# Kernel optimization log

Hardware: AMD Instinct MI355X
Metric: run time of the kernel (lower is better)

## Reference

```python
import jax, jax.numpy as jnp
import numpy as np

VOCAB, EMB, HID = 32000, 512, 1024
L, N = 512, 64


def setup_inputs() -> dict:
    key = jax.random.key(0)
    ks = jax.random.split(key, 10)
    d_in = HID + EMB
    s = 1.0 / np.sqrt(d_in)
    def lin(k):
        kw, kb = jax.random.split(k)
        W = jax.random.uniform(kw, (d_in, HID), jnp.float32, -s, s)
        b = jax.random.uniform(kb, (HID,), jnp.float32, -s, s)
        return W, b
    Wi, bi = lin(ks[0])
    Wf, bf = lin(ks[1])
    Wc, bc = lin(ks[2])
    Wo, bo = lin(ks[3])
    emb = jax.random.normal(ks[4], (VOCAB, EMB), jnp.float32)
    x = jax.random.randint(ks[5], (L, N), 0, VOCAB)
    return {"x": x, "emb": emb, "Wi": Wi, "bi": bi, "Wf": Wf, "bf": bf,
            "Wc": Wc, "bc": bc, "Wo": Wo, "bo": bo}


def reference(x, emb, Wi, bi, Wf, bf, Wc, bc, Wo, bo):
    # x: (L, N) int indices. Embed all timesteps up front (gather), then scan.
    xe = emb[x]  # (L, N, EMB)
    n = x.shape[1]
    h0 = jnp.zeros((n, HID), jnp.float32)
    c0 = jnp.zeros((n, HID), jnp.float32)

    def step(carry, xt):
        h, c = carry
        hx = jnp.concatenate([h, xt], axis=1)  # (N, HID+EMB)
        f = jax.nn.sigmoid(hx @ Wf + bf)
        i = jax.nn.sigmoid(hx @ Wi + bi)
        c_new = f * c + i * jnp.tanh(hx @ Wc + bc)
        o = jax.nn.sigmoid(hx @ Wo + bo)
        h_new = o * jnp.tanh(c_new)
        return (h_new, c_new), h_new

    (_, _), hs = jax.lax.scan(step, (h0, c0), xe)
    return hs  # (L, N, HID)
```

## Files before the change

### kernel.cpp

```cpp
#include <hip/hip_runtime.h>
#include <hip/hip_bf16.h>
#include <cstdint>
#include <cstddef>

typedef unsigned short u16;
typedef __attribute__((ext_vector_type(8))) short short8;
typedef __attribute__((ext_vector_type(4))) float f32x4;

#define L_SEQ 512
#define NB    64
#define HID_  1024
#define EMB_  512
#define DIN   1536
#define NKS   48
#define NKS_H 32
#define ARS   1544
#define HSEQ  (NB * HID_)

__device__ __forceinline__ u16 f2b(float f) {
    uint32_t u = __float_as_uint(f);
    u = (u + 0x7FFFu + ((u >> 16) & 1u)) >> 16;
    return (u16)u;
}

__global__ void pack_w_k(const float* __restrict__ Wi, const float* __restrict__ Wf,
                         const float* __restrict__ Wc, const float* __restrict__ Wo,
                         u16* __restrict__ whxp) {
    int b  = blockIdx.x;
    int ks = b % NKS;
    int gw = (b / NKS) & 3;
    int ug = b / (NKS * 4);
    const float* W = (gw == 0) ? Wi : (gw == 1) ? Wf : (gw == 2) ? Wc : Wo;
    int t  = threadIdx.x;
    int l  = t & 63;
    int ep = t >> 6;
    int k   = ks * 32 + ((l >> 4) * 8) + ep * 2;
    int col = ug * 16 + (l & 15);
    float v0 = W[(size_t)k * HID_ + col];
    float v1 = W[(size_t)(k + 1) * HID_ + col];
    uint32_t pk = (uint32_t)f2b(v0) | ((uint32_t)f2b(v1) << 16);
    size_t dst = (((size_t)b) * 64 + l) * 8 + (size_t)ep * 2;
    *(uint32_t*)(whxp + dst) = pk;
}

__global__ void zero_flags_k(uint32_t* __restrict__ flags) {
    flags[threadIdx.x] = 0u;
}

__global__ __launch_bounds__(256, 1) void lstm_persist_k(
    const u16* __restrict__ whxp, const float* __restrict__ emb,
    const int* __restrict__ x,
    const float* __restrict__ bi, const float* __restrict__ bf_,
    const float* __restrict__ bc, const float* __restrict__ bo,
    u16* __restrict__ hseq, uint32_t* __restrict__ flags,
    float* __restrict__ out)
{
    __shared__ __align__(16) u16 Atile[16][ARS];
    __shared__ float gbuf[4][16][17];

    const int tid = threadIdx.x;
    const int w   = tid >> 6;
    const int l   = tid & 63;
    const int ug  = blockIdx.x & 63;
    const int bj  = blockIdx.x >> 6;
    const int brow0 = bj * 16;

    short8 bw[NKS];
    {
        const short8* bp = (const short8*)whxp + ((size_t)(ug * 4 + w) * NKS) * 64 + l;
        #pragma unroll
        for (int ks = 0; ks < NKS; ++ks) bw[ks] = bp[ks * 64];
    }
    const float* bptr = (w == 0) ? bi : (w == 1) ? bf_ : (w == 2) ? bc : bo;
    const float bias = bptr[ug * 16 + (l & 15)];

    const int erow = tid >> 4;
    const int eu   = tid & 15;
    const size_t cidx = (size_t)(brow0 + erow) * HID_ + (size_t)ug * 16 + eu;
    float creg = 0.f;

    const int grow = tid >> 4;
    const int gc0  = (tid & 15) * 32;

    {
        int token = x[brow0 + grow];
        const float* es = emb + (size_t)token * EMB_ + gc0;
        #pragma unroll
        for (int j = 0; j < 4; ++j) {
            float4 a = *(const float4*)(es + j * 8);
            float4 b = *(const float4*)(es + j * 8 + 4);
            short8 v;
            v[0] = (short)f2b(a.x); v[1] = (short)f2b(a.y);
            v[2] = (short)f2b(a.z); v[3] = (short)f2b(a.w);
            v[4] = (short)f2b(b.x); v[5] = (short)f2b(b.y);
            v[6] = (short)f2b(b.z); v[7] = (short)f2b(b.w);
            *(short8*)(&Atile[grow][1024 + gc0 + j * 8]) = v;
        }
    }
    __syncthreads();

    for (int t = 0; t < L_SEQ; ++t) {
        f32x4 acc0 = {bias, bias, bias, bias};
        f32x4 acc1 = {0.f, 0.f, 0.f, 0.f};
        f32x4 acc2 = {0.f, 0.f, 0.f, 0.f};
        f32x4 acc3 = {0.f, 0.f, 0.f, 0.f};
        const u16* arow = &Atile[l & 15][(l >> 4) * 8];

        #pragma unroll
        for (int ks = NKS_H; ks < NKS; ks += 4) {
            acc0 = __builtin_amdgcn_mfma_f32_16x16x32_bf16(*(const short8*)(arow + ks * 32),        bw[ks],     acc0, 0, 0, 0);
            acc1 = __builtin_amdgcn_mfma_f32_16x16x32_bf16(*(const short8*)(arow + (ks + 1) * 32),  bw[ks + 1], acc1, 0, 0, 0);
            acc2 = __builtin_amdgcn_mfma_f32_16x16x32_bf16(*(const short8*)(arow + (ks + 2) * 32),  bw[ks + 2], acc2, 0, 0, 0);
            acc3 = __builtin_amdgcn_mfma_f32_16x16x32_bf16(*(const short8*)(arow + (ks + 3) * 32),  bw[ks + 3], acc3, 0, 0, 0);
        }
        if (t > 0) {
            #pragma unroll
            for (int ks = 0; ks < NKS_H; ks += 4) {
                acc0 = __builtin_amdgcn_mfma_f32_16x16x32_bf16(*(const short8*)(arow + ks * 32),        bw[ks],     acc0, 0, 0, 0);
                acc1 = __builtin_amdgcn_mfma_f32_16x16x32_bf16(*(const short8*)(arow + (ks + 1) * 32),  bw[ks + 1], acc1, 0, 0, 0);
                acc2 = __builtin_amdgcn_mfma_f32_16x16x32_bf16(*(const short8*)(arow + (ks + 2) * 32),  bw[ks + 2], acc2, 0, 0, 0);
                acc3 = __builtin_amdgcn_mfma_f32_16x16x32_bf16(*(const short8*)(arow + (ks + 3) * 32),  bw[ks + 3], acc3, 0, 0, 0);
            }
        }
        {
            int col = l & 15, rg = l >> 4;
            #pragma unroll
            for (int r = 0; r < 4; ++r)
                gbuf[w][rg * 4 + r][col] = (acc0[r] + acc1[r]) + (acc2[r] + acc3[r]);
        }
        __syncthreads();

        {
            float gi = gbuf[0][erow][eu];
            float gf = gbuf[1][erow][eu];
            float gc = gbuf[2][erow][eu];
            float go = gbuf[3][erow][eu];
            float fi = 1.f / (1.f + __expf(-gi));
            float ff = 1.f / (1.f + __expf(-gf));
            float fo = 1.f / (1.f + __expf(-go));
            float tc = 1.f - 2.f / (__expf(2.f * gc) + 1.f);
            float cn = ff * creg + fi * tc;
            float th = 1.f - 2.f / (__expf(2.f * cn) + 1.f);
            float hn = fo * th;
            creg = cn;
            out[(size_t)t * (NB * HID_) + cidx] = hn;
            __hip_atomic_store(hseq + (size_t)t * HSEQ + cidx, f2b(hn),
                               __ATOMIC_RELAXED, __HIP_MEMORY_SCOPE_AGENT);
        }

        if (t + 1 < L_SEQ) {
            asm volatile("s_waitcnt vmcnt(0)" ::: "memory");
            __syncthreads();
            if (tid == 0)
                __hip_atomic_store(&flags[bj * 64 + ug], (uint32_t)(t + 1),
                                   __ATOMIC_RELAXED, __HIP_MEMORY_SCOPE_AGENT);

            short8 xv[4];
            {
                int token = x[(t + 1) * NB + brow0 + grow];
                const float* es = emb + (size_t)token * EMB_ + gc0;
                #pragma unroll
                for (int j = 0; j < 4; ++j) {
                    float4 a = *(const float4*)(es + j * 8);
                    float4 b = *(const float4*)(es + j * 8 + 4);
                    short8 v;
                    v[0] = (short)f2b(a.x); v[1] = (short)f2b(a.y);
                    v[2] = (short)f2b(a.z); v[3] = (short)f2b(a.w);
                    v[4] = (short)f2b(b.x); v[5] = (short)f2b(b.y);
                    v[6] = (short)f2b(b.z); v[7] = (short)f2b(b.w);
                    xv[j] = v;
                }
            }

            if (tid < 64) {
                for (;;) {
                    uint32_t f = __hip_atomic_load(&flags[bj * 64 + tid],
                                                   __ATOMIC_RELAXED, __HIP_MEMORY_SCOPE_AGENT);
                    if (__all(f > (uint32_t)t)) break;
                    __builtin_amdgcn_s_sleep(2);
                }
            }
            __syncthreads();

            uint4 hv[8];
            {
                const uint32_t* hsrc = (const uint32_t*)(hseq + (size_t)t * HSEQ);
                #pragma unroll
                for (int it = 0; it < 8; ++it) {
                    int i = tid * 4 + it * 1024;
                    hv[it] = *(const uint4*)(hsrc + (size_t)(brow0 + (i >> 9)) * 512 + (i & 511));
                }
            }
            #pragma unroll
            for (int j = 0; j < 4; ++j)
                *(short8*)(&Atile[grow][1024 + gc0 + j * 8]) = xv[j];
            #pragma unroll
            for (int it = 0; it < 8; ++it) {
                int i = tid * 4 + it * 1024;
                *(uint4*)(&Atile[i >> 9][(i & 511) * 2]) = hv[it];
            }
            __syncthreads();
        }
    }
}

extern "C" void kernel_launch(void* const* d_in, const int* in_sizes, int n_in,
                              void* d_out, int out_size, void* d_ws, size_t ws_size,
                              hipStream_t stream) {
    const int*   x   = (const int*)d_in[0];
    const float* emb = (const float*)d_in[1];
    const float* Wi  = (const float*)d_in[2];
    const float* bi  = (const float*)d_in[3];
    const float* Wf  = (const float*)d_in[4];
    const float* bf  = (const float*)d_in[5];
    const float* Wc  = (const float*)d_in[6];
    const float* bc  = (const float*)d_in[7];
    const float* Wo  = (const float*)d_in[8];
    const float* bo  = (const float*)d_in[9];
    float* out = (float*)d_out;

    char* ws = (char*)d_ws;
    u16*      whxp  = (u16*)ws;
    uint32_t* flags = (uint32_t*)(ws + 12582912);
    u16*      hseq  = (u16*)(ws + 12582912 + 4096);

    pack_w_k<<<64 * 4 * NKS, 256, 0, stream>>>(Wi, Wf, Wc, Wo, whxp);
    zero_flags_k<<<1, 256, 0, stream>>>(flags);

    lstm_persist_k<<<256, 256, 0, stream>>>(whxp, emb, x, bi, bf, bc, bo,
                                            hseq, flags, out);
}
```

Before: 2.854 ms.

## Split K across waves, share A fragment across four gates, swizzle LDS

Each wave now owns a quarter of the K dimension for all four gates instead of one gate over full K. Each A fragment load from LDS feeds four MFMAs, which cuts LDS read traffic by four. The four partial sums are reduced through an enlarged gbuf, with bias added in the elementwise stage. The A tile uses an XOR swizzle instead of padding to avoid bank conflicts. The h part is zero-initialized and the t>0 skip is dropped, so step 0 does the full K. The embedding write is moved before the spin-wait, and the sleep interval is shortened.

```diff
diff --git a/kernel.cpp b/kernel.cpp
--- a/kernel.cpp
+++ b/kernel.cpp
@@ -11,10 +11,8 @@
 #define NB    64
 #define HID_  1024
 #define EMB_  512
-#define DIN   1536
 #define NKS   48
-#define NKS_H 32
-#define ARS   1544
+#define KQ_N  12
 #define HSEQ  (NB * HID_)
 
 __device__ __forceinline__ u16 f2b(float f) {
@@ -47,7 +45,9 @@
     flags[threadIdx.x] = 0u;
 }
 
-__global__ __launch_bounds__(256, 1) void lstm_persist_k(
+__global__ __launch_bounds__(256)
+__attribute__((amdgpu_waves_per_eu(1, 1)))
+void lstm_persist_k(
     const u16* __restrict__ whxp, const float* __restrict__ emb,
     const int* __restrict__ x,
     const float* __restrict__ bi, const float* __restrict__ bf_,
@@ -55,86 +55,104 @@
     u16* __restrict__ hseq, uint32_t* __restrict__ flags,
     float* __restrict__ out)
 {
-    __shared__ __align__(16) u16 Atile[16][ARS];
-    __shared__ float gbuf[4][16][17];
+    __shared__ __align__(16) u16 As[16 * 1536];
+    __shared__ float gbuf[4][4][16][16];
 
     const int tid = threadIdx.x;
-    const int w   = tid >> 6;
+    const int kq  = tid >> 6;
     const int l   = tid & 63;
     const int ug  = blockIdx.x & 63;
     const int bj  = blockIdx.x >> 6;
     const int brow0 = bj * 16;
 
-    short8 bw[NKS];
+    short8 bw0[KQ_N], bw1[KQ_N], bw2[KQ_N], bw3[KQ_N];
     {
-        const short8* bp = (const short8*)whxp + ((size_t)(ug * 4 + w) * NKS) * 64 + l;
-        #pragma unroll
-        for (int ks = 0; ks < NKS; ++ks) bw[ks] = bp[ks * 64];
+        const short8* bp = (const short8*)whxp + ((size_t)(ug * 4) * NKS) * 64 + l;
+        #pragma unroll
+        for (int j = 0; j < KQ_N; ++j) {
+            bw0[j] = bp[(0 * NKS + kq * KQ_N + j) * 64];
+            bw1[j] = bp[(1 * NKS + kq * KQ_N + j) * 64];
+            bw2[j] = bp[(2 * NKS + kq * KQ_N + j) * 64];
+            bw3[j] = bp[(3 * NKS + kq * KQ_N + j) * 64];
+        }
     }
-    const float* bptr = (w == 0) ? bi : (w == 1) ? bf_ : (w == 2) ? bc : bo;
-    const float bias = bptr[ug * 16 + (l & 15)];
+
+    const int arow = l & 15;
+    const int aq   = l >> 4;
+    const int k7   = arow & 7;
 
     const int erow = tid >> 4;
     const int eu   = tid & 15;
     const size_t cidx = (size_t)(brow0 + erow) * HID_ + (size_t)ug * 16 + eu;
+    const float bias_i = bi[ug * 16 + eu];
+    const float bias_f = bf_[ug * 16 + eu];
+    const float bias_c = bc[ug * 16 + eu];
+    const float bias_o = bo[ug * 16 + eu];
     float creg = 0.f;
 
     const int grow = tid >> 4;
-    const int gc0  = (tid & 15) * 32;
+    const int gx   = tid & 15;
 
     {
+        uint4 z = make_uint4(0u, 0u, 0u, 0u);
+        #pragma unroll
+        for (int it = 0; it < 8; ++it) {
+            int gidx = tid + it * 256;
+            int r_ = gidx >> 7, gr = gidx & 127;
+            *(uint4*)(&As[r_ * 1536 + (((gr ^ (r_ & 7))) << 3)]) = z;
+        }
         int token = x[brow0 + grow];
-        const float* es = emb + (size_t)token * EMB_ + gc0;
-        #pragma unroll
-        for (int j = 0; j < 4; ++j) {
-            float4 a = *(const float4*)(es + j * 8);
-            float4 b = *(const float4*)(es + j * 8 + 4);
+        const float* es = emb + (size_t)token * EMB_ + gx * 32;
+        #pragma unroll
+        for (int jj = 0; jj < 4; ++jj) {
+            float4 a = *(const float4*)(es + jj * 8);
+            float4 b = *(const float4*)(es + jj * 8 + 4);
             short8 v;
             v[0] = (short)f2b(a.x); v[1] = (short)f2b(a.y);
             v[2] = (short)f2b(a.z); v[3] = (short)f2b(a.w);
             v[4] = (short)f2b(b.x); v[5] = (short)f2b(b.y);
             v[6] = (short)f2b(b.z); v[7] = (short)f2b(b.w);
-            *(short8*)(&Atile[grow][1024 + gc0 + j * 8]) = v;
+            int gr = 128 + gx * 4 + jj;
+            *(short8*)(&As[grow * 1536 + ((gr ^ (grow & 7)) << 3)]) = v;
         }
     }
     __syncthreads();
 
     for (int t = 0; t < L_SEQ; ++t) {
-        f32x4 acc0 = {bias, bias, bias, bias};
-        f32x4 acc1 = {0.f, 0.f, 0.f, 0.f};
-        f32x4 acc2 = {0.f, 0.f, 0.f, 0.f};
-        f32x4 acc3 = {0.f, 0.f, 0.f, 0.f};
-        const u16* arow = &Atile[l & 15][(l >> 4) * 8];
-
-        #pragma unroll
-        for (int ks = NKS_H; ks < NKS; ks += 4) {
-            acc0 = __builtin_amdgcn_mfma_f32_16x16x32_bf16(*(const short8*)(arow + ks * 32),        bw[ks],     acc0, 0, 0, 0);
-            acc1 = __builtin_amdgcn_mfma_f32_16x16x32_bf16(*(const short8*)(arow + (ks + 1) * 32),  bw[ks + 1], acc1, 0, 0, 0);
-            acc2 = __builtin_amdgcn_mfma_f32_16x16x32_bf16(*(const short8*)(arow + (ks + 2) * 32),  bw[ks + 2], acc2, 0, 0, 0);
-            acc3 = __builtin_amdgcn_mfma_f32_16x16x32_bf16(*(const short8*)(arow + (ks + 3) * 32),  bw[ks + 3], acc3, 0, 0, 0);
-        }
-        if (t > 0) {
-            #pragma unroll
-            for (int ks = 0; ks < NKS_H; ks += 4) {
-                acc0 = __builtin_amdgcn_mfma_f32_16x16x32_bf16(*(const short8*)(arow + ks * 32),        bw[ks],     acc0, 0, 0, 0);
-                acc1 = __builtin_amdgcn_mfma_f32_16x16x32_bf16(*(const short8*)(arow + (ks + 1) * 32),  bw[ks + 1], acc1, 0, 0, 0);
-                acc2 = __builtin_amdgcn_mfma_f32_16x16x32_bf16(*(const short8*)(arow + (ks + 2) * 32),  bw[ks + 2], acc2, 0, 0, 0);
-                acc3 = __builtin_amdgcn_mfma_f32_16x16x32_bf16(*(const short8*)(arow + (ks + 3) * 32),  bw[ks + 3], acc3, 0, 0, 0);
-            }
+        f32x4 p0 = {0.f, 0.f, 0.f, 0.f};
+        f32x4 p1 = {0.f, 0.f, 0.f, 0.f};
+        f32x4 p2 = {0.f, 0.f, 0.f, 0.f};
+        f32x4 p3 = {0.f, 0.f, 0.f, 0.f};
+        #pragma unroll
+        for (int j = 0; j < KQ_N; ++j) {
+            int gr = (kq * KQ_N + j) * 4 + aq;
+            short8 av = *(const short8*)(&As[arow * 1536 + ((gr ^ k7) << 3)]);
+            p0 = __builtin_amdgcn_mfma_f32_16x16x32_bf16(av, bw0[j], p0, 0, 0, 0);
+            p1 = __builtin_amdgcn_mfma_f32_16x16x32_bf16(av, bw1[j], p1, 0, 0, 0);
+            p2 = __builtin_amdgcn_mfma_f32_16x16x32_bf16(av, bw2[j], p2, 0, 0, 0);
+            p3 = __builtin_amdgcn_mfma_f32_16x16x32_bf16(av, bw3[j], p3, 0, 0, 0);
         }
         {
             int col = l & 15, rg = l >> 4;
             #pragma unroll
-            for (int r = 0; r < 4; ++r)
-                gbuf[w][rg * 4 + r][col] = (acc0[r] + acc1[r]) + (acc2[r] + acc3[r]);
+            for (int r = 0; r < 4; ++r) {
+                gbuf[kq][0][rg * 4 + r][col] = p0[r];
+                gbuf[kq][1][rg * 4 + r][col] = p1[r];
+                gbuf[kq][2][rg * 4 + r][col] = p2[r];
+                gbuf[kq][3][rg * 4 + r][col] = p3[r];
+            }
         }
         __syncthreads();
 
         {
-            float gi = gbuf[0][erow][eu];
-            float gf = gbuf[1][erow][eu];
-            float gc = gbuf[2][erow][eu];
-            float go = gbuf[3][erow][eu];
+            float gi = ((gbuf[0][0][erow][eu] + gbuf[1][0][erow][eu]) +
+                        (gbuf[2][0][erow][eu] + gbuf[3][0][erow][eu])) + bias_i;
+            float gf = ((gbuf[0][1][erow][eu] + gbuf[1][1][erow][eu]) +
+                        (gbuf[2][1][erow][eu] + gbuf[3][1][erow][eu])) + bias_f;
+            float gc = ((gbuf[0][2][erow][eu] + gbuf[1][2][erow][eu]) +
+                        (gbuf[2][2][erow][eu] + gbuf[3][2][erow][eu])) + bias_c;
+            float go = ((gbuf[0][3][erow][eu] + gbuf[1][3][erow][eu]) +
+                        (gbuf[2][3][erow][eu] + gbuf[3][3][erow][eu])) + bias_o;
             float fi = 1.f / (1.f + __expf(-gi));
             float ff = 1.f / (1.f + __expf(-gf));
             float fo = 1.f / (1.f + __expf(-go));
@@ -155,49 +173,48 @@
                 __hip_atomic_store(&flags[bj * 64 + ug], (uint32_t)(t + 1),
                                    __ATOMIC_RELAXED, __HIP_MEMORY_SCOPE_AGENT);
 
-            short8 xv[4];
             {
                 int token = x[(t + 1) * NB + brow0 + grow];
-                const float* es = emb + (size_t)token * EMB_ + gc0;
-                #pragma unroll
-                for (int j = 0; j < 4; ++j) {
-                    float4 a = *(const float4*)(es + j * 8);
-                    float4 b = *(const float4*)(es + j * 8 + 4);
+                const float* es = emb + (size_t)token * EMB_ + gx * 32;
+                float4 ea[8];
+                #pragma unroll
+                for (int jj = 0; jj < 8; ++jj) ea[jj] = *(const float4*)(es + jj * 4);
+                #pragma unroll
+                for (int jj = 0; jj < 4; ++jj) {
+                    float4 a = ea[jj * 2], b = ea[jj * 2 + 1];
                     short8 v;
                     v[0] = (short)f2b(a.x); v[1] = (short)f2b(a.y);
                     v[2] = (short)f2b(a.z); v[3] = (short)f2b(a.w);
                     v[4] = (short)f2b(b.x); v[5] = (short)f2b(b.y);
                     v[6] = (short)f2b(b.z); v[7] = (short)f2b(b.w);
-                    xv[j] = v;
+                    int gr = 128 + gx * 4 + jj;
+                    *(short8*)(&As[grow * 1536 + ((gr ^ (grow & 7)) << 3)]) = v;
                 }
             }
 
             if (tid < 64) {
                 for (;;) {
-                    uint32_t f = __hip_atomic_load(&flags[bj * 64 + tid],
+                    uint32_t f = __hip_atomic_load(&flags[bj * 64 + l],
                                                    __ATOMIC_RELAXED, __HIP_MEMORY_SCOPE_AGENT);
                     if (__all(f > (uint32_t)t)) break;
-                    __builtin_amdgcn_s_sleep(2);
+                    __builtin_amdgcn_s_sleep(1);
                 }
             }
             __syncthreads();
 
-            uint4 hv[8];
             {
-                const uint32_t* hsrc = (const uint32_t*)(hseq + (size_t)t * HSEQ);
+                const uint4* hsrc = (const uint4*)(hseq + (size_t)t * HSEQ +
+                                                   (size_t)brow0 * HID_);
+                uint4 hv[8];
+                #pragma unroll
+                for (int it = 0; it < 8; ++it) hv[it] = hsrc[it * 256 + tid];
                 #pragma unroll
                 for (int it = 0; it < 8; ++it) {
-                    int i = tid * 4 + it * 1024;
-                    hv[it] = *(const uint4*)(hsrc + (size_t)(brow0 + (i >> 9)) * 512 + (i & 511));
+                    int f16 = (it * 256 + tid) * 8;
+                    int r_  = f16 >> 10;
+                    int gr  = (f16 & 1023) >> 3;
+                    *(uint4*)(&As[r_ * 1536 + ((gr ^ (r_ & 7)) << 3)]) = hv[it];
                 }
-            }
-            #pragma unroll
-            for (int j = 0; j < 4; ++j)
-                *(short8*)(&Atile[grow][1024 + gc0 + j * 8]) = xv[j];
-            #pragma unroll
-            for (int it = 0; it < 8; ++it) {
-                int i = tid * 4 + it * 1024;
-                *(uint4*)(&Atile[i >> 9][(i & 511) * 2]) = hv[it];
             }
             __syncthreads();
         }
```

Result: faster. 2.724 ms (-4.5%).
